# Optimization experiments

Hardware: AMD Instinct MI355X
Metric: run time of the kernel (lower is better)

## Reference

```python
import jax, jax.numpy as jnp
import numpy as np

VOCAB, EMBED, HIDDEN = 32000, 128, 128
LN_EPS = 1e-5
NEG = -1e30

def _layernorm(x, w, b):
    m = jnp.mean(x, axis=-1, keepdims=True)
    v = jnp.mean((x - m) ** 2, axis=-1, keepdims=True)
    return (x - m) * jax.lax.rsqrt(v + LN_EPS) * w + b

def _encode(ids, mask, emb, W1, b1, W2, b2, lnw, lnb):
    x = emb[ids]                                   # [B, L, EMBED]
    h = _layernorm(jax.nn.relu(x @ W1 + b1), lnw, lnb)
    h = _layernorm(jax.nn.relu(h @ W2 + b2), lnw, lnb)  # extra layer (num_layers=2)
    return h * mask[..., None].astype(h.dtype)

def setup_inputs() -> dict:
    key = jax.random.key(0)
    ks = jax.random.split(key, 16)
    s_emb = 1.0
    s_lin = 1.0 / np.sqrt(HIDDEN)
    def lin(k1, k2, din, dout):
        return (jax.random.uniform(k1, (din, dout), jnp.float32, -s_lin, s_lin),
                jax.random.uniform(k2, (dout,), jnp.float32, -s_lin, s_lin))
    q_emb = jax.random.normal(ks[0], (VOCAB, EMBED), jnp.float32).at[0].set(0.0)
    d_emb = jax.random.normal(ks[1], (VOCAB, EMBED), jnp.float32).at[0].set(0.0)
    qW1, qb1 = lin(ks[2], ks[3], EMBED, HIDDEN)
    qW2, qb2 = lin(ks[4], ks[5], HIDDEN, HIDDEN)
    dW1, db1 = lin(ks[6], ks[7], EMBED, HIDDEN)
    dW2, db2 = lin(ks[8], ks[9], HIDDEN, HIDDEN)
    q_lnw = jnp.ones((HIDDEN,), jnp.float32); q_lnb = jnp.zeros((HIDDEN,), jnp.float32)
    d_lnw = jnp.ones((HIDDEN,), jnp.float32); d_lnb = jnp.zeros((HIDDEN,), jnp.float32)
    query_ids = jax.random.randint(ks[10], (64, 64), 0, VOCAB, jnp.int32)
    doc_ids = jax.random.randint(ks[11], (64, 4096), 0, VOCAB, jnp.int32)
    query_mask = jnp.ones((64, 64), jnp.int32)
    doc_mask = jnp.ones((64, 4096), jnp.int32)
    return dict(query_ids=query_ids, doc_ids=doc_ids, query_mask=query_mask, doc_mask=doc_mask,
                q_emb=q_emb, qW1=qW1, qb1=qb1, qW2=qW2, qb2=qb2, q_lnw=q_lnw, q_lnb=q_lnb,
                d_emb=d_emb, dW1=dW1, db1=db1, dW2=dW2, db2=db2, d_lnw=d_lnw, d_lnb=d_lnb)

def reference(query_ids, doc_ids, query_mask, doc_mask,
              q_emb, qW1, qb1, qW2, qb2, q_lnw, q_lnb,
              d_emb, dW1, db1, dW2, db2, d_lnw, d_lnb):
    qv = _encode(query_ids, query_mask, q_emb, qW1, qb1, qW2, qb2, q_lnw, q_lnb)  # [B,Q,H]
    dv = _encode(doc_ids, doc_mask, d_emb, dW1, db1, dW2, db2, d_lnw, d_lnb)      # [B,D,H]
    sim = jnp.einsum('bqh,bdh->bqd', qv, dv)
    sim = sim + (1.0 - doc_mask[:, None, :].astype(sim.dtype)) * NEG
    return jnp.max(sim, axis=2).sum(axis=1)  # [B]
```

## Files before the change

### kernel.cpp

```cpp
#include <hip/hip_runtime.h>

typedef _Float16 f16;
typedef __attribute__((ext_vector_type(8))) _Float16 f16x8;
typedef __attribute__((ext_vector_type(4))) float f32x4;

#define XS 136
#define NEGV (-1e30f)


__device__ __forceinline__ void gl_lds16(const f16* g, f16* l) {
  __builtin_amdgcn_global_load_lds(
      (const __attribute__((address_space(1))) unsigned int*)(g),
      (__attribute__((address_space(3))) unsigned int*)(l), 16, 0, 0);
}

__device__ __forceinline__ void stage_w_full(const f16* __restrict__ Wf,
                                             f16* Ws, int wave, int lane) {
#pragma unroll
  for (int c = 0; c < 8; ++c) {
    int chunk = wave * 8 + c;
    gl_lds16(Wf + chunk * 512 + lane * 8, Ws + chunk * 512);
  }
}

__device__ __forceinline__ void emb_to_xs(const float* __restrict__ row_src,
                                          f16* Xs, int myrow, int seg) {
  const float4* src = (const float4*)(row_src + seg * 32);
  f16x8* dst = (f16x8*)(Xs + myrow * XS + seg * 32);
#pragma unroll
  for (int i = 0; i < 4; ++i) {
    float4 v0 = src[2 * i], v1 = src[2 * i + 1];
    f16x8 o;
    o[0] = (f16)v0.x; o[1] = (f16)v0.y; o[2] = (f16)v0.z; o[3] = (f16)v0.w;
    o[4] = (f16)v1.x; o[5] = (f16)v1.y; o[6] = (f16)v1.z; o[7] = (f16)v1.w;
    dst[i] = o;
  }
}

__device__ __forceinline__ void load_afrag(f16x8* afrag, const f16* Xs,
                                           int wave, int lane) {
  const int r = lane & 15, quad = lane >> 4;
#pragma unroll
  for (int k = 0; k < 4; ++k)
    afrag[k] = *(const f16x8*)(Xs + (wave * 16 + r) * XS + quad * 8 + k * 32);
}

__device__ __forceinline__ void layer_mfma_lds(f32x4* acc, const f16x8* afrag,
                                               const f16* Ws, int lane) {
  const f16* Wl = Ws + lane * 8;
#pragma unroll
  for (int nt = 0; nt < 8; ++nt) {
    f32x4 c = {0.f, 0.f, 0.f, 0.f};
#pragma unroll
    for (int k = 0; k < 4; ++k) {
      f16x8 b = *(const f16x8*)(Wl + (nt * 4 + k) * 512);
      c = __builtin_amdgcn_mfma_f32_16x16x32_f16(afrag[k], b, c, 0, 0, 0);
    }
    acc[nt] = c;
  }
}

__device__ __forceinline__ void epilogue_ln(f32x4* acc, int wave, int lane, f16* Xs,
                                            const float* __restrict__ bias,
                                            const float* __restrict__ lnw,
                                            const float* __restrict__ lnb) {
  const int r = lane & 15, quad = lane >> 4;
  float s1[4] = {0, 0, 0, 0}, s2[4] = {0, 0, 0, 0};
#pragma unroll
  for (int nt = 0; nt < 8; ++nt) {
    float bv = bias[nt * 16 + r];
#pragma unroll
    for (int g = 0; g < 4; ++g) {
      float z = fmaxf(acc[nt][g] + bv, 0.f);
      acc[nt][g] = z; s1[g] += z; s2[g] += z * z;
    }
  }
#pragma unroll
  for (int off = 1; off < 16; off <<= 1) {
#pragma unroll
    for (int g = 0; g < 4; ++g) {
      s1[g] += __shfl_xor(s1[g], off);
      s2[g] += __shfl_xor(s2[g], off);
    }
  }
  float mean[4], rstd[4];
#pragma unroll
  for (int g = 0; g < 4; ++g) {
    mean[g] = s1[g] * (1.f / 128.f);
    rstd[g] = rsqrtf(s2[g] * (1.f / 128.f) - mean[g] * mean[g] + 1e-5f);
  }
#pragma unroll
  for (int nt = 0; nt < 8; ++nt) {
    float w = lnw[nt * 16 + r], bb = lnb[nt * 16 + r];
#pragma unroll
    for (int g = 0; g < 4; ++g) {
      float h = (acc[nt][g] - mean[g]) * rstd[g] * w + bb;
      Xs[(wave * 16 + quad * 4 + g) * XS + nt * 16 + r] = (f16)h;
    }
  }
}


__global__ __launch_bounds__(256) void prep_kernel(
    const float* __restrict__ qW1, const float* __restrict__ qW2,
    const float* __restrict__ dW1, const float* __restrict__ dW2,
    f16* __restrict__ out) {
  int mat = blockIdx.x >> 3;
  int blk = blockIdx.x & 7;
  const float* W = mat == 0 ? qW1 : mat == 1 ? qW2 : mat == 2 ? dW1 : dW2;
  int u = blk * 256 + threadIdx.x;
  int r = u & 15, quad = (u >> 4) & 3, k = (u >> 6) & 3, nt = u >> 8;
  const float* src = W + (k * 32 + quad * 8) * 128 + nt * 16 + r;
  f16x8 o;
#pragma unroll
  for (int j = 0; j < 8; ++j) o[j] = (f16)src[j * 128];
  *(f16x8*)(out + (size_t)mat * 16384 + (size_t)u * 8) = o;
}

__global__ __launch_bounds__(256) void encode_kernel(
    const int* __restrict__ qids, const int* __restrict__ qmask,
    const float* __restrict__ q_emb, const float* __restrict__ d_emb,
    const f16* __restrict__ qW1f, const float* __restrict__ qb1,
    const f16* __restrict__ qW2f, const float* __restrict__ qb2,
    const float* __restrict__ q_lnw, const float* __restrict__ q_lnb,
    const f16* __restrict__ dW1f, const float* __restrict__ db1,
    const f16* __restrict__ dW2f, const float* __restrict__ db2,
    const float* __restrict__ d_lnw, const float* __restrict__ d_lnb,
    f16* __restrict__ qv, f16* __restrict__ dvt) {
  __shared__ __align__(16) f16 Xs[64 * XS];
  __shared__ __align__(16) f16 Ws[16384];
  const int tid = threadIdx.x, wave = tid >> 6, lane = tid & 63;
  const int myrow = tid >> 2, seg = tid & 3;
  const bool dside = blockIdx.x < 500;
  const int b = dside ? 0 : blockIdx.x - 500;
  const int v0 = blockIdx.x * 64;

  const f16* W1f = dside ? dW1f : qW1f;
  const f16* W2f = dside ? dW2f : qW2f;
  const float* b1 = dside ? db1 : qb1;
  const float* b2 = dside ? db2 : qb2;
  const float* lnw = dside ? d_lnw : q_lnw;
  const float* lnb = dside ? d_lnb : q_lnb;

  stage_w_full(W1f, Ws, wave, lane);
  if (dside) emb_to_xs(d_emb + (size_t)(v0 + myrow) * 128, Xs, myrow, seg);
  else       emb_to_xs(q_emb + (size_t)qids[b * 64 + myrow] * 128, Xs, myrow, seg);
  __syncthreads();
  f32x4 acc[8];
  f16x8 afrag[4];
  load_afrag(afrag, Xs, wave, lane);
  layer_mfma_lds(acc, afrag, Ws, lane);
  __syncthreads();
  stage_w_full(W2f, Ws, wave, lane);
  epilogue_ln(acc, wave, lane, Xs, b1, lnw, lnb);
  __syncthreads();
  load_afrag(afrag, Xs, wave, lane);
  layer_mfma_lds(acc, afrag, Ws, lane);
  epilogue_ln(acc, wave, lane, Xs, b2, lnw, lnb);
  if (dside) {
    f16x8* dst = (f16x8*)(dvt + (size_t)(v0 + myrow) * 128 + seg * 32);
    const f16x8* src = (const f16x8*)(Xs + myrow * XS + seg * 32);
#pragma unroll
    for (int i = 0; i < 4; ++i) dst[i] = src[i];
    return;
  }
  __syncthreads();
#pragma unroll
  for (int i = 0; i < 4; ++i) {
    int u = tid + i * 256;
    int r = u & 15, quad = (u >> 4) & 3, k = (u >> 6) & 3, mt = u >> 8;
    int row = mt * 16 + r;
    f16 m = (f16)(float)qmask[b * 64 + row];
    f16x8 v = *(const f16x8*)(Xs + row * XS + k * 32 + quad * 8);
#pragma unroll
    for (int j = 0; j < 8; ++j) v[j] = v[j] * m;
    *(f16x8*)(qv + (size_t)b * 8192 + (size_t)u * 8) = v;
  }
}

__global__ __launch_bounds__(256) void docsim_kernel(
    const int* __restrict__ dids, const int* __restrict__ dmask,
    const f16* __restrict__ dvt, const f16* __restrict__ qv,
    float* __restrict__ partials) {
  __shared__ __align__(16) f16 Xs[64 * XS];
  const int tid = threadIdx.x, wave = tid >> 6, lane = tid & 63;
  const int b = blockIdx.x >> 4;
  const int dc0 = (blockIdx.x & 15) * 4;
  const int myrow = tid >> 2, seg = tid & 3;
  const int r = lane & 15, quad = lane >> 4;
  f16x8 qfrag[4];
#pragma unroll
  for (int k = 0; k < 4; ++k) {
    int u = (wave * 4 + k) * 64 + quad * 16 + r;
    qfrag[k] = *(const f16x8*)(qv + (size_t)b * 8192 + (size_t)u * 8);
  }
  int myid[4];
#pragma unroll
  for (int c = 0; c < 4; ++c)
    myid[c] = dids[(size_t)b * 4096 + (dc0 + c) * 64 + myrow];
#pragma unroll
  for (int c = 0; c < 4; ++c) {
    const int dc = dc0 + c;
    float mv[4];
#pragma unroll
    for (int nt = 0; nt < 4; ++nt)
      mv[nt] = (float)dmask[(size_t)b * 4096 + dc * 64 + nt * 16 + r];
    f16x8 row[4];
    {
      const f16x8* src = (const f16x8*)(dvt + (size_t)myid[c] * 128 + seg * 32);
#pragma unroll
      for (int i = 0; i < 4; ++i) row[i] = src[i];
    }
    if (c) __syncthreads();
    {
      f16x8* dst = (f16x8*)(Xs + myrow * XS + seg * 32);
#pragma unroll
      for (int i = 0; i < 4; ++i) dst[i] = row[i];
    }
    __syncthreads();
    float rowmax[4] = {NEGV, NEGV, NEGV, NEGV};
#pragma unroll
    for (int nt = 0; nt < 4; ++nt) {
      f32x4 cc = {0.f, 0.f, 0.f, 0.f};
#pragma unroll
      for (int k = 0; k < 4; ++k) {
        f16x8 bfrag = *(const f16x8*)(Xs + (nt * 16 + r) * XS + quad * 8 + k * 32);
        cc = __builtin_amdgcn_mfma_f32_16x16x32_f16(qfrag[k], bfrag, cc, 0, 0, 0);
      }
#pragma unroll
      for (int g = 0; g < 4; ++g) {
        float v = (mv[nt] != 0.f) ? cc[g] : NEGV;
        rowmax[g] = fmaxf(rowmax[g], v);
      }
    }
#pragma unroll
    for (int off = 1; off < 16; off <<= 1) {
#pragma unroll
      for (int g = 0; g < 4; ++g)
        rowmax[g] = fmaxf(rowmax[g], __shfl_xor(rowmax[g], off));
    }
    if (r == 0) {
#pragma unroll
      for (int g = 0; g < 4; ++g) {
        int q = wave * 16 + quad * 4 + g;
        partials[((size_t)b * 64 + q) * 64 + dc] = rowmax[g];
      }
    }
  }
}

__global__ __launch_bounds__(256) void reduce_kernel(
    const float* __restrict__ partials, float* __restrict__ out) {
  __shared__ float red[64][4];
  const int b = blockIdx.x, tid = threadIdx.x;
  const int q = tid >> 2, seg = tid & 3;
  const float4* p = (const float4*)(partials + ((size_t)b * 64 + q) * 64 + seg * 16);
  float m = NEGV;
#pragma unroll
  for (int i = 0; i < 4; ++i) {
    float4 v = p[i];
    m = fmaxf(m, fmaxf(fmaxf(v.x, v.y), fmaxf(v.z, v.w)));
  }
  red[q][seg] = m;
  __syncthreads();
  if (tid < 64) {
    float qm = fmaxf(fmaxf(red[tid][0], red[tid][1]), fmaxf(red[tid][2], red[tid][3]));
    float s = qm;
#pragma unroll
    for (int off = 1; off < 64; off <<= 1) s += __shfl_xor(s, off);
    if (tid == 0) out[b] = s;
  }
}


extern "C" void kernel_launch(void* const* d_in, const int* in_sizes, int n_in,
                              void* d_out, int out_size, void* d_ws, size_t ws_size,
                              hipStream_t stream) {
  const int* query_ids  = (const int*)d_in[0];
  const int* doc_ids    = (const int*)d_in[1];
  const int* query_mask = (const int*)d_in[2];
  const int* doc_mask   = (const int*)d_in[3];
  const float* q_emb = (const float*)d_in[4];
  const float* qW1 = (const float*)d_in[5];
  const float* qb1 = (const float*)d_in[6];
  const float* qW2 = (const float*)d_in[7];
  const float* qb2 = (const float*)d_in[8];
  const float* q_lnw = (const float*)d_in[9];
  const float* q_lnb = (const float*)d_in[10];
  const float* d_emb = (const float*)d_in[11];
  const float* dW1 = (const float*)d_in[12];
  const float* db1 = (const float*)d_in[13];
  const float* dW2 = (const float*)d_in[14];
  const float* db2 = (const float*)d_in[15];
  const float* d_lnw = (const float*)d_in[16];
  const float* d_lnb = (const float*)d_in[17];

  char* ws = (char*)d_ws;
  f16* wts  = (f16*)(ws + 0);
  f16* qW1f = wts;
  f16* qW2f = wts + 16384;
  f16* dW1f = wts + 32768;
  f16* dW2f = wts + 49152;
  f16* dvt = (f16*)(ws + 131072);
  f16* qv  = (f16*)(ws + 131072 + 8192000);
  float* partials = (float*)(ws + 131072 + 8192000 + 1048576);
  float* out = (float*)d_out;

  prep_kernel<<<32, 256, 0, stream>>>(qW1, qW2, dW1, dW2, wts);
  encode_kernel<<<564, 256, 0, stream>>>(query_ids, query_mask, q_emb, d_emb,
                                         qW1f, qb1, qW2f, qb2, q_lnw, q_lnb,
                                         dW1f, db1, dW2f, db2, d_lnw, d_lnb,
                                         qv, dvt);
  docsim_kernel<<<1024, 256, 0, stream>>>(doc_ids, doc_mask, dvt, qv, partials);
  reduce_kernel<<<64, 256, 0, stream>>>(partials, out);
}
```

Before: 134.5 us.

## Load doc fragments directly from global and fuse final reduction via last-block counter

The docsim kernel no longer stages gathered doc rows through LDS with barriers. Each lane now loads its MFMA B-fragment straight from the gathered embedding table, with ids and masks prefetched up front. The separate reduce kernel is folded into docsim: an atomic per-batch counter picks the last block, which does the max/sum reduction. This removes a kernel launch and LDS syncs, but adds a memset, atomics, threadfences and uncoalesced 16-byte gathers from global memory.

After: 290.1 us. 116% more time.

```diff
diff --git a/kernel.cpp b/kernel.cpp
--- a/kernel.cpp
+++ b/kernel.cpp
@@ -181,12 +181,13 @@
 __global__ __launch_bounds__(256) void docsim_kernel(
     const int* __restrict__ dids, const int* __restrict__ dmask,
     const f16* __restrict__ dvt, const f16* __restrict__ qv,
-    float* __restrict__ partials) {
-  __shared__ __align__(16) f16 Xs[64 * XS];
+    float* __restrict__ partials, int* __restrict__ counters,
+    float* __restrict__ out) {
+  __shared__ float red[256];
+  __shared__ int lastflag;
   const int tid = threadIdx.x, wave = tid >> 6, lane = tid & 63;
   const int b = blockIdx.x >> 4;
   const int dc0 = (blockIdx.x & 15) * 4;
-  const int myrow = tid >> 2, seg = tid & 3;
   const int r = lane & 15, quad = lane >> 4;
   f16x8 qfrag[4];
 #pragma unroll
@@ -194,42 +195,31 @@
     int u = (wave * 4 + k) * 64 + quad * 16 + r;
     qfrag[k] = *(const f16x8*)(qv + (size_t)b * 8192 + (size_t)u * 8);
   }
-  int myid[4];
-#pragma unroll
-  for (int c = 0; c < 4; ++c)
-    myid[c] = dids[(size_t)b * 4096 + (dc0 + c) * 64 + myrow];
+  int id[4][4];
+  float mv[4][4];
 #pragma unroll
   for (int c = 0; c < 4; ++c) {
-    const int dc = dc0 + c;
-    float mv[4];
-#pragma unroll
-    for (int nt = 0; nt < 4; ++nt)
-      mv[nt] = (float)dmask[(size_t)b * 4096 + dc * 64 + nt * 16 + r];
-    f16x8 row[4];
-    {
-      const f16x8* src = (const f16x8*)(dvt + (size_t)myid[c] * 128 + seg * 32);
-#pragma unroll
-      for (int i = 0; i < 4; ++i) row[i] = src[i];
-    }
-    if (c) __syncthreads();
-    {
-      f16x8* dst = (f16x8*)(Xs + myrow * XS + seg * 32);
-#pragma unroll
-      for (int i = 0; i < 4; ++i) dst[i] = row[i];
-    }
-    __syncthreads();
+    const int base = b * 4096 + (dc0 + c) * 64;
+#pragma unroll
+    for (int nt = 0; nt < 4; ++nt) {
+      id[c][nt] = dids[base + nt * 16 + r];
+      mv[c][nt] = (float)dmask[base + nt * 16 + r];
+    }
+  }
+#pragma unroll
+  for (int c = 0; c < 4; ++c) {
     float rowmax[4] = {NEGV, NEGV, NEGV, NEGV};
 #pragma unroll
     for (int nt = 0; nt < 4; ++nt) {
       f32x4 cc = {0.f, 0.f, 0.f, 0.f};
 #pragma unroll
       for (int k = 0; k < 4; ++k) {
-        f16x8 bfrag = *(const f16x8*)(Xs + (nt * 16 + r) * XS + quad * 8 + k * 32);
+        f16x8 bfrag = *(const f16x8*)(dvt + (size_t)id[c][nt] * 128 + k * 32 + quad * 8);
         cc = __builtin_amdgcn_mfma_f32_16x16x32_f16(qfrag[k], bfrag, cc, 0, 0, 0);
       }
 #pragma unroll
       for (int g = 0; g < 4; ++g) {
-        float v = (mv[nt] != 0.f) ? cc[g] : NEGV;
+        float v = (mv[c][nt] != 0.f) ? cc[g] : NEGV;
         rowmax[g] = fmaxf(rowmax[g], v);
       }
     }
@@ -243,32 +233,34 @@
 #pragma unroll
       for (int g = 0; g < 4; ++g) {
         int q = wave * 16 + quad * 4 + g;
-        partials[((size_t)b * 64 + q) * 64 + dc] = rowmax[g];
+        partials[((size_t)b * 64 + q) * 64 + dc0 + c] = rowmax[g];
       }
     }
   }
-}
-
-__global__ __launch_bounds__(256) void reduce_kernel(
-    const float* __restrict__ partials, float* __restrict__ out) {
-  __shared__ float red[64][4];
-  const int b = blockIdx.x, tid = threadIdx.x;
-  const int q = tid >> 2, seg = tid & 3;
-  const float4* p = (const float4*)(partials + ((size_t)b * 64 + q) * 64 + seg * 16);
-  float m = NEGV;
-#pragma unroll
-  for (int i = 0; i < 4; ++i) {
-    float4 v = p[i];
-    m = fmaxf(m, fmaxf(fmaxf(v.x, v.y), fmaxf(v.z, v.w)));
-  }
-  red[q][seg] = m;
+  __threadfence();
+  if (tid == 0) lastflag = (atomicAdd(&counters[b], 1) == 15);
+  __syncthreads();
+  if (!lastflag) return;
+  __threadfence();
+  {
+    int q = tid >> 2, s = tid & 3;
+    const float4* p = (const float4*)(partials + ((size_t)b * 64 + q) * 64 + s * 16);
+    float m = NEGV;
+#pragma unroll
+    for (int i = 0; i < 4; ++i) {
+      float4 v = p[i];
+      m = fmaxf(m, fmaxf(fmaxf(v.x, v.y), fmaxf(v.z, v.w)));
+    }
+    red[q * 4 + s] = m;
+  }
   __syncthreads();
   if (tid < 64) {
-    float qm = fmaxf(fmaxf(red[tid][0], red[tid][1]), fmaxf(red[tid][2], red[tid][3]));
-    float s = qm;
-#pragma unroll
-    for (int off = 1; off < 64; off <<= 1) s += __shfl_xor(s, off);
-    if (tid == 0) out[b] = s;
+    float qm = fmaxf(fmaxf(red[tid * 4], red[tid * 4 + 1]),
+                     fmaxf(red[tid * 4 + 2], red[tid * 4 + 3]));
+    float sum = qm;
+#pragma unroll
+    for (int off = 1; off < 64; off <<= 1) sum += __shfl_xor(sum, off);
+    if (tid == 0) out[b] = sum;
   }
 }
 
@@ -304,13 +296,15 @@
   f16* dvt = (f16*)(ws + 131072);
   f16* qv  = (f16*)(ws + 131072 + 8192000);
   float* partials = (float*)(ws + 131072 + 8192000 + 1048576);
+  int* counters   = (int*)(ws + 131072 + 8192000 + 2097152);
   float* out = (float*)d_out;
 
+  hipMemsetAsync(counters, 0, 64 * sizeof(int), stream);
   prep_kernel<<<32, 256, 0, stream>>>(qW1, qW2, dW1, dW2, wts);
   encode_kernel<<<564, 256, 0, stream>>>(query_ids, query_mask, q_emb, d_emb,
                                          qW1f, qb1, qW2f, qb2, q_lnw, q_lnb,
                                          dW1f, db1, dW2f, db2, d_lnw, d_lnb,
                                          qv, dvt);
-  docsim_kernel<<<1024, 256, 0, stream>>>(doc_ids, doc_mask, dvt, qv, partials);
-  reduce_kernel<<<64, 256, 0, stream>>>(partials, out);
-}
+  docsim_kernel<<<1024, 256, 0, stream>>>(doc_ids, doc_mask, dvt, qv,
+                                          partials, counters, out);
+}
```
